# Optimization experiments

Measured on AMD Instinct MI355X. Metric: run time of the kernel, lower is better.

Reference implementation:

```python
import jax, jax.numpy as jnp
import numpy as np

B, T, F = 256, 288, 64
UNITS = [128, 64, 64, 32]
SCALE = 0.05  # small init so relu-activated recurrence stays numerically stable


def _lstm_scan(x_tbf, Wk, Wr, b):
    """Keras LSTM with activation=relu, recurrent_activation=sigmoid.
    x_tbf: [T, B, in]. Returns all hidden states [T, B, u].
    Gate order in the fused kernel is (i, f, g, o), as in Keras."""
    u = Wr.shape[0]
    bsz = x_tbf.shape[1]

    def step(carry, xt):
        h, c = carry
        z = xt @ Wk + h @ Wr + b            # [B, 4u]
        i, f, g, o = jnp.split(z, 4, axis=-1)
        i = jax.nn.sigmoid(i)
        f = jax.nn.sigmoid(f)
        g = jax.nn.relu(g)                   # cell-input activation = relu
        o = jax.nn.sigmoid(o)
        c = f * c + i * g
        h = o * jax.nn.relu(c)               # output activation = relu
        return (h, c), h

    init = (jnp.zeros((bsz, u), x_tbf.dtype), jnp.zeros((bsz, u), x_tbf.dtype))
    _, hs = jax.lax.scan(step, init, x_tbf)
    return hs  # [T, B, u]


def setup_inputs() -> dict:
    key = jax.random.key(0)
    ks = jax.random.split(key, 20)
    out = {"x": jax.random.normal(ks[0], (B, T, F), dtype=jnp.float32)}
    ins = [F] + UNITS[:-1]
    ki = 1
    for li, (din, u) in enumerate(zip(ins, UNITS), start=1):
        out[f"W{li}"] = jax.random.normal(ks[ki], (din, 4 * u), jnp.float32) * SCALE; ki += 1
        out[f"U{li}"] = jax.random.normal(ks[ki], (u, 4 * u), jnp.float32) * SCALE; ki += 1
        out[f"b{li}"] = jnp.zeros((4 * u,), jnp.float32)
    out["Wf"] = jax.random.normal(ks[ki], (UNITS[-1], 16), jnp.float32) * SCALE; ki += 1
    out["bf"] = jnp.zeros((16,), jnp.float32)
    out["Wo"] = jax.random.normal(ks[ki], (16, 1), jnp.float32) * SCALE
    out["bo"] = jnp.zeros((1,), jnp.float32)
    return out


def reference(x, W1, U1, b1, W2, U2, b2, W3, U3, b3, W4, U4, b4, Wf, bf, Wo, bo):
    # Dropout layers are identity at inference (Keras deterministic call).
    h = jnp.transpose(x, (1, 0, 2))          # [T, B, F] time-major for scan
    h = _lstm_scan(h, W1, U1, b1)            # [T, B, 128]
    h = _lstm_scan(h, W2, U2, b2)            # [T, B, 64]
    h = _lstm_scan(h, W3, U3, b3)            # [T, B, 64]
    h_last = _lstm_scan(h, W4, U4, b4)[-1]   # [B, 32] (return_sequences=False)
    fc = jax.nn.relu(h_last @ Wf + bf)       # [B, 16]
    return fc @ Wo + bo                      # [B, 1]
```

## Files before the change

kernel.cpp:

```cpp
#include <hip/hip_runtime.h>
#include <math.h>

#define TSTEPS 288
#define NTHREADS 512

typedef float f32x2 __attribute__((ext_vector_type(2)));

__device__ __forceinline__ float sigmoidf_(float x) {
    return 1.0f / (1.0f + __expf(-x));
}

__device__ __forceinline__ void pkfma(f32x2& acc, f32x2 w, f32x2 x) {
    asm("v_pk_fma_f32 %0, %1, %2, %0" : "+v"(acc) : "v"(w), "v"(x));
}

template<int NS>
__device__ __forceinline__ float allreduce_seg(float v) {
    if constexpr (NS > 1)
        v += __int_as_float(__builtin_amdgcn_update_dpp(
                0, __float_as_int(v), 0xB1, 0xF, 0xF, true));
    if constexpr (NS > 2)
        v += __int_as_float(__builtin_amdgcn_update_dpp(
                0, __float_as_int(v), 0x4E, 0xF, 0xF, true));
    if constexpr (NS > 4)
        v += __int_as_float(__builtin_amdgcn_ds_swizzle(
                __float_as_int(v), 0x101F));
    return v;
}

template<int NS, int KSEG>
__device__ __forceinline__ int perm_idx(int j) {
    return (((j % KSEG) >> 2) * NS + (j / KSEG)) * 4 + (j & 3);
}

__device__ void run_l1(const float* __restrict__ Wk, const float* __restrict__ Wr,
                       const float* __restrict__ bias, const float* __restrict__ xg,
                       float* __restrict__ seq, float* __restrict__ xh,
                       float* __restrict__ xring, int tid)
{
    constexpr int U = 128, COLS = 512, NPI = 8, NPH = 16, NP = NPI + NPH;
    const int seg = tid & 3;
    const int u   = tid >> 2;

    f32x2 w[4][NP];
#pragma unroll
    for (int q = 0; q < NPI; ++q) {
        const int k0 = seg * 16 + 2 * q;
#pragma unroll
        for (int g = 0; g < 4; ++g)
            w[g][q] = f32x2{Wk[(size_t)k0 * COLS + g * U + u],
                            Wk[(size_t)(k0 + 1) * COLS + g * U + u]};
    }
#pragma unroll
    for (int q = 0; q < NPH; ++q) {
        const int k0 = seg * 32 + 2 * q;
#pragma unroll
        for (int g = 0; g < 4; ++g)
            w[g][NPI + q] = f32x2{Wr[(size_t)k0 * COLS + g * U + u],
                                  Wr[(size_t)(k0 + 1) * COLS + g * U + u]};
    }
    float bz[4];
#pragma unroll
    for (int g = 0; g < 4; ++g) bz[g] = bias[g * U + u];
#pragma unroll
    for (int g = 0; g < 4; ++g)
#pragma unroll
        for (int q = 0; q < NP; ++q)
            asm volatile("" : "+v"(w[g][q]));

    float cst = 0.0f;

    for (int t = 0; t < TSTEPS; ++t) {
        const float* __restrict__ xr = xh + (t & 1) * 128;
        float* __restrict__ xw       = xh + ((t + 1) & 1) * 128;

        float xstage = 0.0f;
        if (tid < 64 && (t + 1) < TSTEPS) xstage = xg[(t + 1) * 64 + tid];

        f32x2 ac0 = {0.f,0.f}, ac1 = {0.f,0.f}, ac2 = {0.f,0.f}, ac3 = {0.f,0.f};

        {
            const float4* in4 = reinterpret_cast<const float4*>(xring + (t & 1) * 64) + seg;
#pragma unroll
            for (int k = 0; k < 4; ++k) {
                const float4 v = in4[k * 4];
                const f32x2 lo = {v.x, v.y}, hi = {v.z, v.w};
                pkfma(ac0, w[0][2*k],   lo); pkfma(ac0, w[0][2*k+1], hi);
                pkfma(ac1, w[1][2*k],   lo); pkfma(ac1, w[1][2*k+1], hi);
                pkfma(ac2, w[2][2*k],   lo); pkfma(ac2, w[2][2*k+1], hi);
                pkfma(ac3, w[3][2*k],   lo); pkfma(ac3, w[3][2*k+1], hi);
            }
        }
        {
            const float4* h4 = reinterpret_cast<const float4*>(xr) + seg;
#pragma unroll
            for (int k = 0; k < 8; ++k) {
                const float4 v = h4[k * 4];
                const f32x2 lo = {v.x, v.y}, hi = {v.z, v.w};
                const int pb = NPI + 2 * k;
                pkfma(ac0, w[0][pb], lo); pkfma(ac0, w[0][pb+1], hi);
                pkfma(ac1, w[1][pb], lo); pkfma(ac1, w[1][pb+1], hi);
                pkfma(ac2, w[2][pb], lo); pkfma(ac2, w[2][pb+1], hi);
                pkfma(ac3, w[3][pb], lo); pkfma(ac3, w[3][pb+1], hi);
            }
        }
        float a0 = allreduce_seg<4>(ac0[0] + ac0[1]) + bz[0];
        float a1 = allreduce_seg<4>(ac1[0] + ac1[1]) + bz[1];
        float a2 = allreduce_seg<4>(ac2[0] + ac2[1]) + bz[2];
        float a3 = allreduce_seg<4>(ac3[0] + ac3[1]) + bz[3];

        const float gi = sigmoidf_(a0);
        const float gf = sigmoidf_(a1);
        const float gg = fmaxf(a2, 0.0f);
        const float go = sigmoidf_(a3);
        cst = fmaf(gf, cst, gi * gg);
        const float h = go * fmaxf(cst, 0.0f);

        if (seg == 0) {
            const int pj = perm_idx<4, 32>(u);
            xw[pj] = h;
            seq[t * 128 + pj] = h;
        }
        if (tid < 64 && (t + 1) < TSTEPS)
            xring[((t + 1) & 1) * 64 + perm_idx<4, 16>(tid)] = xstage;
        __syncthreads();
    }
}

__device__ void fused_l2(const float* __restrict__ Wk, const float* __restrict__ Wr,
                         const float* __restrict__ bias,
                         const float* __restrict__ seq, float* __restrict__ xh2,
                         int lt)
{
    constexpr int U = 64, COLS = 256, NPI = 16, NPH = 8, NP = NPI + NPH;
    const int seg = lt & 3;
    const int u   = lt >> 2;

    f32x2 w[4][NP];
#pragma unroll
    for (int q = 0; q < NPI; ++q) {
        const int k0 = seg * 32 + 2 * q;
#pragma unroll
        for (int g = 0; g < 4; ++g)
            w[g][q] = f32x2{Wk[(size_t)k0 * COLS + g * U + u],
                            Wk[(size_t)(k0 + 1) * COLS + g * U + u]};
    }
#pragma unroll
    for (int q = 0; q < NPH; ++q) {
        const int k0 = seg * 16 + 2 * q;
#pragma unroll
        for (int g = 0; g < 4; ++g)
            w[g][NPI + q] = f32x2{Wr[(size_t)k0 * COLS + g * U + u],
                                  Wr[(size_t)(k0 + 1) * COLS + g * U + u]};
    }
    float bz[4];
#pragma unroll
    for (int g = 0; g < 4; ++g) bz[g] = bias[g * U + u];
#pragma unroll
    for (int g = 0; g < 4; ++g)
#pragma unroll
        for (int q = 0; q < NP; ++q)
            asm volatile("" : "+v"(w[g][q]));

    float cst = 0.0f;

    for (int i = 0; i < TSTEPS + 2; ++i) {
        if (i < TSTEPS) {
            f32x2 ac0 = {0.f,0.f}, ac1 = {0.f,0.f}, ac2 = {0.f,0.f}, ac3 = {0.f,0.f};
            {
                const float4* in4 = reinterpret_cast<const float4*>(seq + i * 128) + seg;
#pragma unroll
                for (int k = 0; k < 8; ++k) {
                    const float4 v = in4[k * 4];
                    const f32x2 lo = {v.x, v.y}, hi = {v.z, v.w};
                    pkfma(ac0, w[0][2*k],   lo); pkfma(ac0, w[0][2*k+1], hi);
                    pkfma(ac1, w[1][2*k],   lo); pkfma(ac1, w[1][2*k+1], hi);
                    pkfma(ac2, w[2][2*k],   lo); pkfma(ac2, w[2][2*k+1], hi);
                    pkfma(ac3, w[3][2*k],   lo); pkfma(ac3, w[3][2*k+1], hi);
                }
            }
            {
                const float4* h4 = reinterpret_cast<const float4*>(xh2 + ((i + 1) & 1) * 64) + seg;
#pragma unroll
                for (int k = 0; k < 4; ++k) {
                    const float4 v = h4[k * 4];
                    const f32x2 lo = {v.x, v.y}, hi = {v.z, v.w};
                    const int pb = NPI + 2 * k;
                    pkfma(ac0, w[0][pb], lo); pkfma(ac0, w[0][pb+1], hi);
                    pkfma(ac1, w[1][pb], lo); pkfma(ac1, w[1][pb+1], hi);
                    pkfma(ac2, w[2][pb], lo); pkfma(ac2, w[2][pb+1], hi);
                    pkfma(ac3, w[3][pb], lo); pkfma(ac3, w[3][pb+1], hi);
                }
            }
            float a0 = allreduce_seg<4>(ac0[0] + ac0[1]) + bz[0];
            float a1 = allreduce_seg<4>(ac1[0] + ac1[1]) + bz[1];
            float a2 = allreduce_seg<4>(ac2[0] + ac2[1]) + bz[2];
            float a3 = allreduce_seg<4>(ac3[0] + ac3[1]) + bz[3];

            const float gi = sigmoidf_(a0);
            const float gf = sigmoidf_(a1);
            const float gg = fmaxf(a2, 0.0f);
            const float go = sigmoidf_(a3);
            cst = fmaf(gf, cst, gi * gg);
            const float h = go * fmaxf(cst, 0.0f);

            if (seg == 0) xh2[(i & 1) * 64 + perm_idx<4, 16>(u)] = h;
        }
        __syncthreads();
    }
}

__device__ void fused_l34(const float* __restrict__ W3k, const float* __restrict__ W3r,
                          const float* __restrict__ b3,
                          const float* __restrict__ W4k, const float* __restrict__ W4r,
                          const float* __restrict__ b4,
                          const float* __restrict__ xh2, float* __restrict__ xh3,
                          float* __restrict__ xh4, int lt)
{
    const int seg3 = lt & 3,  u3 = lt >> 2;
    const int seg4 = lt & 7,  u4 = lt >> 3;

    f32x2 w3[4][16];
#pragma unroll
    for (int q = 0; q < 8; ++q) {
        const int k0 = seg3 * 16 + 2 * q;
#pragma unroll
        for (int g = 0; g < 4; ++g)
            w3[g][q] = f32x2{W3k[(size_t)k0 * 256 + g * 64 + u3],
                             W3k[(size_t)(k0 + 1) * 256 + g * 64 + u3]};
    }
#pragma unroll
    for (int q = 0; q < 8; ++q) {
        const int k0 = seg3 * 16 + 2 * q;
#pragma unroll
        for (int g = 0; g < 4; ++g)
            w3[g][8 + q] = f32x2{W3r[(size_t)k0 * 256 + g * 64 + u3],
                                 W3r[(size_t)(k0 + 1) * 256 + g * 64 + u3]};
    }
    f32x2 w4[4][6];
#pragma unroll
    for (int q = 0; q < 4; ++q) {
        const int k0 = seg4 * 8 + 2 * q;
#pragma unroll
        for (int g = 0; g < 4; ++g)
            w4[g][q] = f32x2{W4k[(size_t)k0 * 128 + g * 32 + u4],
                             W4k[(size_t)(k0 + 1) * 128 + g * 32 + u4]};
    }
#pragma unroll
    for (int q = 0; q < 2; ++q) {
        const int k0 = seg4 * 4 + 2 * q;
#pragma unroll
        for (int g = 0; g < 4; ++g)
            w4[g][4 + q] = f32x2{W4r[(size_t)k0 * 128 + g * 32 + u4],
                                 W4r[(size_t)(k0 + 1) * 128 + g * 32 + u4]};
    }
    float bz3[4], bz4[4];
#pragma unroll
    for (int g = 0; g < 4; ++g) { bz3[g] = b3[g * 64 + u3]; bz4[g] = b4[g * 32 + u4]; }
#pragma unroll
    for (int g = 0; g < 4; ++g) {
#pragma unroll
        for (int q = 0; q < 16; ++q) asm volatile("" : "+v"(w3[g][q]));
#pragma unroll
        for (int q = 0; q < 6;  ++q) asm volatile("" : "+v"(w4[g][q]));
    }

    float c3 = 0.0f, c4 = 0.0f;

    for (int i = 0; i < TSTEPS + 2; ++i) {
        if (i >= 1 && i <= TSTEPS) {
            f32x2 ac0 = {0.f,0.f}, ac1 = {0.f,0.f}, ac2 = {0.f,0.f}, ac3 = {0.f,0.f};
            {
                const float4* in4 = reinterpret_cast<const float4*>(xh2 + ((i - 1) & 1) * 64) + seg3;
#pragma unroll
                for (int k = 0; k < 4; ++k) {
                    const float4 v = in4[k * 4];
                    const f32x2 lo = {v.x, v.y}, hi = {v.z, v.w};
                    pkfma(ac0, w3[0][2*k],   lo); pkfma(ac0, w3[0][2*k+1], hi);
                    pkfma(ac1, w3[1][2*k],   lo); pkfma(ac1, w3[1][2*k+1], hi);
                    pkfma(ac2, w3[2][2*k],   lo); pkfma(ac2, w3[2][2*k+1], hi);
                    pkfma(ac3, w3[3][2*k],   lo); pkfma(ac3, w3[3][2*k+1], hi);
                }
            }
            {
                const float4* h4 = reinterpret_cast<const float4*>(xh3 + (i & 1) * 64) + seg3;
#pragma unroll
                for (int k = 0; k < 4; ++k) {
                    const float4 v = h4[k * 4];
                    const f32x2 lo = {v.x, v.y}, hi = {v.z, v.w};
                    const int pb = 8 + 2 * k;
                    pkfma(ac0, w3[0][pb], lo); pkfma(ac0, w3[0][pb+1], hi);
                    pkfma(ac1, w3[1][pb], lo); pkfma(ac1, w3[1][pb+1], hi);
                    pkfma(ac2, w3[2][pb], lo); pkfma(ac2, w3[2][pb+1], hi);
                    pkfma(ac3, w3[3][pb], lo); pkfma(ac3, w3[3][pb+1], hi);
                }
            }
            float a0 = allreduce_seg<4>(ac0[0] + ac0[1]) + bz3[0];
            float a1 = allreduce_seg<4>(ac1[0] + ac1[1]) + bz3[1];
            float a2 = allreduce_seg<4>(ac2[0] + ac2[1]) + bz3[2];
            float a3 = allreduce_seg<4>(ac3[0] + ac3[1]) + bz3[3];
            const float gi = sigmoidf_(a0);
            const float gf = sigmoidf_(a1);
            const float gg = fmaxf(a2, 0.0f);
            const float go = sigmoidf_(a3);
            c3 = fmaf(gf, c3, gi * gg);
            const float h = go * fmaxf(c3, 0.0f);
            if (seg3 == 0) xh3[((i - 1) & 1) * 64 + perm_idx<4, 16>(u3)] = h;
        }
        if (i >= 2) {
            f32x2 ac0 = {0.f,0.f}, ac1 = {0.f,0.f}, ac2 = {0.f,0.f}, ac3 = {0.f,0.f};
            {
                const float4* in4 = reinterpret_cast<const float4*>(xh3 + (i & 1) * 64);
#pragma unroll
                for (int k = 0; k < 2; ++k) {
                    const float4 v = in4[((seg4 & 1) * 2 + k) * 4 + (seg4 >> 1)];
                    const f32x2 lo = {v.x, v.y}, hi = {v.z, v.w};
                    pkfma(ac0, w4[0][2*k],   lo); pkfma(ac0, w4[0][2*k+1], hi);
                    pkfma(ac1, w4[1][2*k],   lo); pkfma(ac1, w4[1][2*k+1], hi);
                    pkfma(ac2, w4[2][2*k],   lo); pkfma(ac2, w4[2][2*k+1], hi);
                    pkfma(ac3, w4[3][2*k],   lo); pkfma(ac3, w4[3][2*k+1], hi);
                }
            }
            {
                const float4 v = reinterpret_cast<const float4*>(xh4 + ((i - 1) & 1) * 32)[seg4];
                const f32x2 lo = {v.x, v.y}, hi = {v.z, v.w};
                pkfma(ac0, w4[0][4], lo); pkfma(ac0, w4[0][5], hi);
                pkfma(ac1, w4[1][4], lo); pkfma(ac1, w4[1][5], hi);
                pkfma(ac2, w4[2][4], lo); pkfma(ac2, w4[2][5], hi);
                pkfma(ac3, w4[3][4], lo); pkfma(ac3, w4[3][5], hi);
            }
            float a0 = allreduce_seg<8>(ac0[0] + ac0[1]) + bz4[0];
            float a1 = allreduce_seg<8>(ac1[0] + ac1[1]) + bz4[1];
            float a2 = allreduce_seg<8>(ac2[0] + ac2[1]) + bz4[2];
            float a3 = allreduce_seg<8>(ac3[0] + ac3[1]) + bz4[3];
            const float gi = sigmoidf_(a0);
            const float gf = sigmoidf_(a1);
            const float gg = fmaxf(a2, 0.0f);
            const float go = sigmoidf_(a3);
            c4 = fmaf(gf, c4, gi * gg);
            const float h = go * fmaxf(c4, 0.0f);
            if (seg4 == 0) xh4[(i & 1) * 32 + u4] = h;
        }
        __syncthreads();
    }
}

extern "C" __global__ void __launch_bounds__(NTHREADS, 2)
lstm_stack_kernel(const float* __restrict__ x,
                  const float* __restrict__ W1, const float* __restrict__ U1, const float* __restrict__ b1,
                  const float* __restrict__ W2, const float* __restrict__ U2, const float* __restrict__ b2,
                  const float* __restrict__ W3, const float* __restrict__ U3, const float* __restrict__ b3,
                  const float* __restrict__ W4, const float* __restrict__ U4, const float* __restrict__ b4,
                  const float* __restrict__ Wf, const float* __restrict__ bf,
                  const float* __restrict__ Wo, const float* __restrict__ bo,
                  float* __restrict__ out)
{
    __shared__ __align__(16) float seq[TSTEPS * 128];
    __shared__ __align__(16) float xh1[2 * 128];
    __shared__ __align__(16) float xring[2 * 64];
    __shared__ __align__(16) float xh2[2 * 64];
    __shared__ __align__(16) float xh3[2 * 64];
    __shared__ __align__(16) float xh4[2 * 32];
    __shared__ __align__(16) float hbuf[16];

    const int tid = threadIdx.x;
    const float* xg = x + (size_t)blockIdx.x * TSTEPS * 64;

    if (tid < 128) xh1[tid] = 0.0f;
    if (tid < 64) {
        xring[perm_idx<4, 16>(tid)] = xg[tid];
        xh2[64 + tid] = 0.0f;
        xh3[64 + tid] = 0.0f;
    }
    if (tid < 32) xh4[32 + tid] = 0.0f;
    __syncthreads();

    run_l1(W1, U1, b1, xg, seq, xh1, xring, tid);

    if (tid < 256) fused_l2(W2, U2, b2, seq, xh2, tid);
    else           fused_l34(W3, U3, b3, W4, U4, b4, xh2, xh3, xh4, tid - 256);
    __syncthreads();

    if (tid < 16) {
        float acc = bf[tid];
#pragma unroll
        for (int k = 0; k < 32; ++k) acc = fmaf(xh4[32 + k], Wf[k * 16 + tid], acc);
        hbuf[tid] = fmaxf(acc, 0.0f);
    }
    __syncthreads();
    if (tid == 0) {
        float acc = bo[0];
#pragma unroll
        for (int k = 0; k < 16; ++k) acc = fmaf(hbuf[k], Wo[k], acc);
        out[blockIdx.x] = acc;
    }
}

extern "C" void kernel_launch(void* const* d_in, const int* in_sizes, int n_in,
                              void* d_out, int out_size, void* d_ws, size_t ws_size,
                              hipStream_t stream) {
    const float* x  = (const float*)d_in[0];
    const float* W1 = (const float*)d_in[1];
    const float* U1 = (const float*)d_in[2];
    const float* b1 = (const float*)d_in[3];
    const float* W2 = (const float*)d_in[4];
    const float* U2 = (const float*)d_in[5];
    const float* b2 = (const float*)d_in[6];
    const float* W3 = (const float*)d_in[7];
    const float* U3 = (const float*)d_in[8];
    const float* b3 = (const float*)d_in[9];
    const float* W4 = (const float*)d_in[10];
    const float* U4 = (const float*)d_in[11];
    const float* b4 = (const float*)d_in[12];
    const float* Wf = (const float*)d_in[13];
    const float* bf = (const float*)d_in[14];
    const float* Wo = (const float*)d_in[15];
    const float* bo = (const float*)d_in[16];
    float* out = (float*)d_out;

    lstm_stack_kernel<<<dim3(256), dim3(NTHREADS), 0, stream>>>(
        x, W1, U1, b1, W2, U2, b2, W3, U3, b3, W4, U4, b4, Wf, bf, Wo, bo, out);
}
```

Measured before the change: 576.2 us.

## Chunk input projections of layers 1-2 over four timesteps with prepacked weights

A prep kernel repacks W1 and W2 into a per-thread contiguous layout in workspace. The main kernel then computes the input-to-gate projection for four timesteps at once by streaming these weights from global/L2 instead of holding them in registers. Only the recurrent weights stay in registers, which frees VGPRs and takes the input projection out of the per-step critical path. The cost is repeated weight reads from memory each chunk, a larger x staging ring, and an extra kernel launch, with a fallback path kept for when workspace is too small.

```diff
diff --git a/kernel.cpp b/kernel.cpp
--- a/kernel.cpp
+++ b/kernel.cpp
@@ -33,181 +33,247 @@
     return (((j % KSEG) >> 2) * NS + (j / KSEG)) * 4 + (j & 3);
 }
 
-__device__ void run_l1(const float* __restrict__ Wk, const float* __restrict__ Wr,
-                       const float* __restrict__ bias, const float* __restrict__ xg,
-                       float* __restrict__ seq, float* __restrict__ xh,
-                       float* __restrict__ xring, int tid)
+extern "C" __global__ void prep_kernel(const float* __restrict__ W1,
+                                       const float* __restrict__ W2,
+                                       float* __restrict__ ws)
 {
-    constexpr int U = 128, COLS = 512, NPI = 8, NPH = 16, NP = NPI + NPH;
+    const int tid = threadIdx.x;
+    {
+        const int u = tid >> 2, seg = tid & 3;
+#pragma unroll
+        for (int g = 0; g < 4; ++g)
+#pragma unroll
+            for (int kk = 0; kk < 16; ++kk)
+                ws[tid * 64 + g * 16 + kk] = W1[(seg * 16 + kk) * 512 + g * 128 + u];
+    }
+    if (tid < 256) {
+        const int u = tid >> 2, seg = tid & 3;
+#pragma unroll
+        for (int g = 0; g < 4; ++g)
+#pragma unroll
+            for (int kk = 0; kk < 32; ++kk)
+                ws[32768 + tid * 128 + g * 32 + kk] = W2[(seg * 32 + kk) * 256 + g * 64 + u];
+    }
+}
+
+__device__ void run_l1_chunked(const float* __restrict__ U1w,
+                               const float* __restrict__ bias,
+                               const float* __restrict__ xg,
+                               const float* __restrict__ wsA,
+                               float* __restrict__ seq,
+                               float* __restrict__ xh,
+                               float* __restrict__ xring,
+                               int tid)
+{
     const int seg = tid & 3;
     const int u   = tid >> 2;
 
-    f32x2 w[4][NP];
-#pragma unroll
-    for (int q = 0; q < NPI; ++q) {
-        const int k0 = seg * 16 + 2 * q;
-#pragma unroll
-        for (int g = 0; g < 4; ++g)
-            w[g][q] = f32x2{Wk[(size_t)k0 * COLS + g * U + u],
-                            Wk[(size_t)(k0 + 1) * COLS + g * U + u]};
-    }
-#pragma unroll
-    for (int q = 0; q < NPH; ++q) {
-        const int k0 = seg * 32 + 2 * q;
-#pragma unroll
-        for (int g = 0; g < 4; ++g)
-            w[g][NPI + q] = f32x2{Wr[(size_t)k0 * COLS + g * U + u],
-                                  Wr[(size_t)(k0 + 1) * COLS + g * U + u]};
+    f32x2 wr[4][16];
+#pragma unroll
+    for (int q = 0; q < 16; ++q) {
+        const int row = seg * 32 + 2 * q;
+#pragma unroll
+        for (int g = 0; g < 4; ++g)
+            wr[g][q] = f32x2{U1w[(size_t)row * 512 + g * 128 + u],
+                             U1w[(size_t)(row + 1) * 512 + g * 128 + u]};
     }
     float bz[4];
 #pragma unroll
-    for (int g = 0; g < 4; ++g) bz[g] = bias[g * U + u];
+    for (int g = 0; g < 4; ++g) bz[g] = bias[g * 128 + u];
 #pragma unroll
     for (int g = 0; g < 4; ++g)
 #pragma unroll
-        for (int q = 0; q < NP; ++q)
-            asm volatile("" : "+v"(w[g][q]));
+        for (int q = 0; q < 16; ++q)
+            asm volatile("" : "+v"(wr[g][q]));
+
+    if (tid < 128) xh[tid] = 0.0f;
+    if (tid < 256) {
+        const int r = tid >> 6, c = tid & 63;
+        xring[r * 64 + c] = xg[r * 64 + c];
+    }
+    __syncthreads();
 
     float cst = 0.0f;
-
-    for (int t = 0; t < TSTEPS; ++t) {
-        const float* __restrict__ xr = xh + (t & 1) * 128;
-        float* __restrict__ xw       = xh + ((t + 1) & 1) * 128;
-
-        float xstage = 0.0f;
-        if (tid < 64 && (t + 1) < TSTEPS) xstage = xg[(t + 1) * 64 + tid];
-
-        f32x2 ac0 = {0.f,0.f}, ac1 = {0.f,0.f}, ac2 = {0.f,0.f}, ac3 = {0.f,0.f};
-
+    const float4* wA = reinterpret_cast<const float4*>(wsA) + tid * 16;
+
+    for (int cc = 0; cc < 72; ++cc) {
+        float zx[4][4];
         {
-            const float4* in4 = reinterpret_cast<const float4*>(xring + (t & 1) * 64) + seg;
-#pragma unroll
-            for (int k = 0; k < 4; ++k) {
-                const float4 v = in4[k * 4];
-                const f32x2 lo = {v.x, v.y}, hi = {v.z, v.w};
-                pkfma(ac0, w[0][2*k],   lo); pkfma(ac0, w[0][2*k+1], hi);
-                pkfma(ac1, w[1][2*k],   lo); pkfma(ac1, w[1][2*k+1], hi);
-                pkfma(ac2, w[2][2*k],   lo); pkfma(ac2, w[2][2*k+1], hi);
-                pkfma(ac3, w[3][2*k],   lo); pkfma(ac3, w[3][2*k+1], hi);
-            }
-        }
-        {
+            const float4* xr4 = reinterpret_cast<const float4*>(xring + (cc & 1) * 256);
+            f32x2 acc2[4][4];
+#pragma unroll
+            for (int t = 0; t < 4; ++t)
+#pragma unroll
+                for (int g = 0; g < 4; ++g) acc2[t][g] = f32x2{0.f, 0.f};
+
+#pragma unroll
+            for (int g = 0; g < 4; ++g) {
+                const float4 w0 = wA[g * 4 + 0], w1 = wA[g * 4 + 1],
+                             w2 = wA[g * 4 + 2], w3 = wA[g * 4 + 3];
+#pragma unroll
+                for (int t = 0; t < 4; ++t) {
+                    const float4 x0 = xr4[t * 16 + seg * 4 + 0];
+                    const float4 x1 = xr4[t * 16 + seg * 4 + 1];
+                    const float4 x2 = xr4[t * 16 + seg * 4 + 2];
+                    const float4 x3 = xr4[t * 16 + seg * 4 + 3];
+                    pkfma(acc2[t][g], f32x2{w0.x, w0.y}, f32x2{x0.x, x0.y});
+                    pkfma(acc2[t][g], f32x2{w0.z, w0.w}, f32x2{x0.z, x0.w});
+                    pkfma(acc2[t][g], f32x2{w1.x, w1.y}, f32x2{x1.x, x1.y});
+                    pkfma(acc2[t][g], f32x2{w1.z, w1.w}, f32x2{x1.z, x1.w});
+                    pkfma(acc2[t][g], f32x2{w2.x, w2.y}, f32x2{x2.x, x2.y});
+                    pkfma(acc2[t][g], f32x2{w2.z, w2.w}, f32x2{x2.z, x2.w});
+                    pkfma(acc2[t][g], f32x2{w3.x, w3.y}, f32x2{x3.x, x3.y});
+                    pkfma(acc2[t][g], f32x2{w3.z, w3.w}, f32x2{x3.z, x3.w});
+                }
+            }
+#pragma unroll
+            for (int t = 0; t < 4; ++t)
+#pragma unroll
+                for (int g = 0; g < 4; ++g)
+                    zx[t][g] = allreduce_seg<4>(acc2[t][g][0] + acc2[t][g][1]);
+        }
+
+#pragma unroll
+        for (int tp = 0; tp < 4; ++tp) {
+            const int t = cc * 4 + tp;
+            const float* __restrict__ xr = xh + (t & 1) * 128;
+            float* __restrict__ xw       = xh + ((t + 1) & 1) * 128;
+
+            f32x2 a2[4] = {f32x2{0.f,0.f}, f32x2{0.f,0.f}, f32x2{0.f,0.f}, f32x2{0.f,0.f}};
             const float4* h4 = reinterpret_cast<const float4*>(xr) + seg;
 #pragma unroll
             for (int k = 0; k < 8; ++k) {
                 const float4 v = h4[k * 4];
                 const f32x2 lo = {v.x, v.y}, hi = {v.z, v.w};
-                const int pb = NPI + 2 * k;
-                pkfma(ac0, w[0][pb], lo); pkfma(ac0, w[0][pb+1], hi);
-                pkfma(ac1, w[1][pb], lo); pkfma(ac1, w[1][pb+1], hi);
-                pkfma(ac2, w[2][pb], lo); pkfma(ac2, w[2][pb+1], hi);
-                pkfma(ac3, w[3][pb], lo); pkfma(ac3, w[3][pb+1], hi);
-            }
-        }
-        float a0 = allreduce_seg<4>(ac0[0] + ac0[1]) + bz[0];
-        float a1 = allreduce_seg<4>(ac1[0] + ac1[1]) + bz[1];
-        float a2 = allreduce_seg<4>(ac2[0] + ac2[1]) + bz[2];
-        float a3 = allreduce_seg<4>(ac3[0] + ac3[1]) + bz[3];
-
-        const float gi = sigmoidf_(a0);
-        const float gf = sigmoidf_(a1);
-        const float gg = fmaxf(a2, 0.0f);
-        const float go = sigmoidf_(a3);
-        cst = fmaf(gf, cst, gi * gg);
-        const float h = go * fmaxf(cst, 0.0f);
-
-        if (seg == 0) {
-            const int pj = perm_idx<4, 32>(u);
-            xw[pj] = h;
-            seq[t * 128 + pj] = h;
-        }
-        if (tid < 64 && (t + 1) < TSTEPS)
-            xring[((t + 1) & 1) * 64 + perm_idx<4, 16>(tid)] = xstage;
-        __syncthreads();
-    }
-}
-
-__device__ void fused_l2(const float* __restrict__ Wk, const float* __restrict__ Wr,
-                         const float* __restrict__ bias,
-                         const float* __restrict__ seq, float* __restrict__ xh2,
-                         int lt)
+                pkfma(a2[0], wr[0][2*k], lo); pkfma(a2[0], wr[0][2*k+1], hi);
+                pkfma(a2[1], wr[1][2*k], lo); pkfma(a2[1], wr[1][2*k+1], hi);
+                pkfma(a2[2], wr[2][2*k], lo); pkfma(a2[2], wr[2][2*k+1], hi);
+                pkfma(a2[3], wr[3][2*k], lo); pkfma(a2[3], wr[3][2*k+1], hi);
+            }
+            float a[4];
+#pragma unroll
+            for (int g = 0; g < 4; ++g)
+                a[g] = allreduce_seg<4>(a2[g][0] + a2[g][1]) + zx[tp][g] + bz[g];
+
+            const float gi = sigmoidf_(a[0]);
+            const float gf = sigmoidf_(a[1]);
+            const float gg = fmaxf(a[2], 0.0f);
+            const float go = sigmoidf_(a[3]);
+            cst = fmaf(gf, cst, gi * gg);
+            const float h = go * fmaxf(cst, 0.0f);
+
+            if (seg == 0) {
+                const int pj = perm_idx<4, 32>(u);
+                xw[pj] = h;
+                seq[t * 128 + pj] = h;
+            }
+            if (tp == 0 && tid < 256) {
+                const int r = (cc + 1) * 4 + (tid >> 6), c = tid & 63;
+                if (r < TSTEPS)
+                    xring[((cc + 1) & 1) * 256 + (tid >> 6) * 64 + c] = xg[r * 64 + c];
+            }
+            __syncthreads();
+        }
+    }
+}
+
+__device__ void fused_l2c(const float* __restrict__ U2w,
+                          const float* __restrict__ bias,
+                          const float* __restrict__ wsB,
+                          const float* __restrict__ seq,
+                          float* __restrict__ xh2,
+                          int lt)
 {
-    constexpr int U = 64, COLS = 256, NPI = 16, NPH = 8, NP = NPI + NPH;
     const int seg = lt & 3;
     const int u   = lt >> 2;
 
-    f32x2 w[4][NP];
-#pragma unroll
-    for (int q = 0; q < NPI; ++q) {
-        const int k0 = seg * 32 + 2 * q;
-#pragma unroll
-        for (int g = 0; g < 4; ++g)
-            w[g][q] = f32x2{Wk[(size_t)k0 * COLS + g * U + u],
-                            Wk[(size_t)(k0 + 1) * COLS + g * U + u]};
-    }
-#pragma unroll
-    for (int q = 0; q < NPH; ++q) {
-        const int k0 = seg * 16 + 2 * q;
-#pragma unroll
-        for (int g = 0; g < 4; ++g)
-            w[g][NPI + q] = f32x2{Wr[(size_t)k0 * COLS + g * U + u],
-                                  Wr[(size_t)(k0 + 1) * COLS + g * U + u]};
+    f32x2 wr[4][8];
+#pragma unroll
+    for (int q = 0; q < 8; ++q) {
+        const int row = seg * 16 + 2 * q;
+#pragma unroll
+        for (int g = 0; g < 4; ++g)
+            wr[g][q] = f32x2{U2w[(size_t)row * 256 + g * 64 + u],
+                             U2w[(size_t)(row + 1) * 256 + g * 64 + u]};
     }
     float bz[4];
 #pragma unroll
-    for (int g = 0; g < 4; ++g) bz[g] = bias[g * U + u];
+    for (int g = 0; g < 4; ++g) bz[g] = bias[g * 64 + u];
 #pragma unroll
     for (int g = 0; g < 4; ++g)
 #pragma unroll
-        for (int q = 0; q < NP; ++q)
-            asm volatile("" : "+v"(w[g][q]));
+        for (int q = 0; q < 8; ++q)
+            asm volatile("" : "+v"(wr[g][q]));
 
     float cst = 0.0f;
-
-    for (int i = 0; i < TSTEPS + 2; ++i) {
-        if (i < TSTEPS) {
-            f32x2 ac0 = {0.f,0.f}, ac1 = {0.f,0.f}, ac2 = {0.f,0.f}, ac3 = {0.f,0.f};
-            {
-                const float4* in4 = reinterpret_cast<const float4*>(seq + i * 128) + seg;
-#pragma unroll
-                for (int k = 0; k < 8; ++k) {
-                    const float4 v = in4[k * 4];
-                    const f32x2 lo = {v.x, v.y}, hi = {v.z, v.w};
-                    pkfma(ac0, w[0][2*k],   lo); pkfma(ac0, w[0][2*k+1], hi);
-                    pkfma(ac1, w[1][2*k],   lo); pkfma(ac1, w[1][2*k+1], hi);
-                    pkfma(ac2, w[2][2*k],   lo); pkfma(ac2, w[2][2*k+1], hi);
-                    pkfma(ac3, w[3][2*k],   lo); pkfma(ac3, w[3][2*k+1], hi);
+    const float4* wB = reinterpret_cast<const float4*>(wsB) + lt * 32;
+
+    for (int cc = 0; cc < 72; ++cc) {
+        float zx[4][4];
+        {
+            f32x2 acc2[4][4];
+#pragma unroll
+            for (int t = 0; t < 4; ++t)
+#pragma unroll
+                for (int g = 0; g < 4; ++g) acc2[t][g] = f32x2{0.f, 0.f};
+
+#pragma unroll
+            for (int g = 0; g < 4; ++g) {
+                float4 wv[8];
+#pragma unroll
+                for (int n = 0; n < 8; ++n) wv[n] = wB[g * 8 + n];
+#pragma unroll
+                for (int t = 0; t < 4; ++t) {
+                    const float4* in4 = reinterpret_cast<const float4*>(
+                        seq + (cc * 4 + t) * 128) + seg;
+#pragma unroll
+                    for (int n = 0; n < 8; ++n) {
+                        const float4 v = in4[n * 4];
+                        pkfma(acc2[t][g], f32x2{wv[n].x, wv[n].y}, f32x2{v.x, v.y});
+                        pkfma(acc2[t][g], f32x2{wv[n].z, wv[n].w}, f32x2{v.z, v.w});
+                    }
                 }
             }
-            {
-                const float4* h4 = reinterpret_cast<const float4*>(xh2 + ((i + 1) & 1) * 64) + seg;
-#pragma unroll
-                for (int k = 0; k < 4; ++k) {
-                    const float4 v = h4[k * 4];
-                    const f32x2 lo = {v.x, v.y}, hi = {v.z, v.w};
-                    const int pb = NPI + 2 * k;
-                    pkfma(ac0, w[0][pb], lo); pkfma(ac0, w[0][pb+1], hi);
-                    pkfma(ac1, w[1][pb], lo); pkfma(ac1, w[1][pb+1], hi);
-                    pkfma(ac2, w[2][pb], lo); pkfma(ac2, w[2][pb+1], hi);
-                    pkfma(ac3, w[3][pb], lo); pkfma(ac3, w[3][pb+1], hi);
-                }
-            }
-            float a0 = allreduce_seg<4>(ac0[0] + ac0[1]) + bz[0];
-            float a1 = allreduce_seg<4>(ac1[0] + ac1[1]) + bz[1];
-            float a2 = allreduce_seg<4>(ac2[0] + ac2[1]) + bz[2];
-            float a3 = allreduce_seg<4>(ac3[0] + ac3[1]) + bz[3];
-
-            const float gi = sigmoidf_(a0);
-            const float gf = sigmoidf_(a1);
-            const float gg = fmaxf(a2, 0.0f);
-            const float go = sigmoidf_(a3);
+#pragma unroll
+            for (int t = 0; t < 4; ++t)
+#pragma unroll
+                for (int g = 0; g < 4; ++g)
+                    zx[t][g] = allreduce_seg<4>(acc2[t][g][0] + acc2[t][g][1]);
+        }
+
+#pragma unroll
+        for (int tp = 0; tp < 4; ++tp) {
+            const int i = cc * 4 + tp;
+            f32x2 a2[4] = {f32x2{0.f,0.f}, f32x2{0.f,0.f}, f32x2{0.f,0.f}, f32x2{0.f,0.f}};
+            const float4* h4 = reinterpret_cast<const float4*>(
+                xh2 + ((i + 1) & 1) * 64) + seg;
+#pragma unroll
+            for (int k = 0; k < 4; ++k) {
+                const float4 v = h4[k * 4];
+                const f32x2 lo = {v.x, v.y}, hi = {v.z, v.w};
+                pkfma(a2[0], wr[0][2*k], lo); pkfma(a2[0], wr[0][2*k+1], hi);
+                pkfma(a2[1], wr[1][2*k], lo); pkfma(a2[1], wr[1][2*k+1], hi);
+                pkfma(a2[2], wr[2][2*k], lo); pkfma(a2[2], wr[2][2*k+1], hi);
+                pkfma(a2[3], wr[3][2*k], lo); pkfma(a2[3], wr[3][2*k+1], hi);
+            }
+            float a[4];
+#pragma unroll
+            for (int g = 0; g < 4; ++g)
+                a[g] = allreduce_seg<4>(a2[g][0] + a2[g][1]) + zx[tp][g] + bz[g];
+
+            const float gi = sigmoidf_(a[0]);
+            const float gf = sigmoidf_(a[1]);
+            const float gg = fmaxf(a[2], 0.0f);
+            const float go = sigmoidf_(a[3]);
             cst = fmaf(gf, cst, gi * gg);
             const float h = go * fmaxf(cst, 0.0f);
 
             if (seg == 0) xh2[(i & 1) * 64 + perm_idx<4, 16>(u)] = h;
-        }
-        __syncthreads();
-    }
+            __syncthreads();
+        }
+    }
+    __syncthreads();
+    __syncthreads();
 }
 
 __device__ void fused_l34(const float* __restrict__ W3k, const float* __restrict__ W3r,
@@ -346,14 +412,237 @@
 }
 
 extern "C" __global__ void __launch_bounds__(NTHREADS, 2)
-lstm_stack_kernel(const float* __restrict__ x,
-                  const float* __restrict__ W1, const float* __restrict__ U1, const float* __restrict__ b1,
-                  const float* __restrict__ W2, const float* __restrict__ U2, const float* __restrict__ b2,
-                  const float* __restrict__ W3, const float* __restrict__ U3, const float* __restrict__ b3,
-                  const float* __restrict__ W4, const float* __restrict__ U4, const float* __restrict__ b4,
-                  const float* __restrict__ Wf, const float* __restrict__ bf,
-                  const float* __restrict__ Wo, const float* __restrict__ bo,
-                  float* __restrict__ out)
+lstm_fast_kernel(const float* __restrict__ x,
+                 const float* __restrict__ U1, const float* __restrict__ b1,
+                 const float* __restrict__ U2, const float* __restrict__ b2,
+                 const float* __restrict__ W3, const float* __restrict__ U3, const float* __restrict__ b3,
+                 const float* __restrict__ W4, const float* __restrict__ U4, const float* __restrict__ b4,
+                 const float* __restrict__ Wf, const float* __restrict__ bf,
+                 const float* __restrict__ Wo, const float* __restrict__ bo,
+                 const float* __restrict__ ws,
+                 float* __restrict__ out)
+{
+    __shared__ __align__(16) float seq[TSTEPS * 128];
+    __shared__ __align__(16) float xh1[2 * 128];
+    __shared__ __align__(16) float xring[2 * 256];
+    __shared__ __align__(16) float xh2[2 * 64];
+    __shared__ __align__(16) float xh3[2 * 64];
+    __shared__ __align__(16) float xh4[2 * 32];
+    __shared__ __align__(16) float hbuf[16];
+
+    const int tid = threadIdx.x;
+    const float* xg = x + (size_t)blockIdx.x * TSTEPS * 64;
+
+    if (tid < 64) { xh2[64 + tid] = 0.0f; xh3[64 + tid] = 0.0f; }
+    if (tid < 32) xh4[32 + tid] = 0.0f;
+
+    run_l1_chunked(U1, b1, xg, ws, seq, xh1, xring, tid);
+    __syncthreads();
+
+    if (tid < 256) fused_l2c(U2, b2, ws + 32768, seq, xh2, tid);
+    else           fused_l34(W3, U3, b3, W4, U4, b4, xh2, xh3, xh4, tid - 256);
+    __syncthreads();
+
+    if (tid < 16) {
+        float acc = bf[tid];
+#pragma unroll
+        for (int k = 0; k < 32; ++k) acc = fmaf(xh4[32 + k], Wf[k * 16 + tid], acc);
+        hbuf[tid] = fmaxf(acc, 0.0f);
+    }
+    __syncthreads();
+    if (tid == 0) {
+        float acc = bo[0];
+#pragma unroll
+        for (int k = 0; k < 16; ++k) acc = fmaf(hbuf[k], Wo[k], acc);
+        out[blockIdx.x] = acc;
+    }
+}
+
+__device__ void run_l1_fb(const float* __restrict__ Wk, const float* __restrict__ Wr,
+                          const float* __restrict__ bias, const float* __restrict__ xg,
+                          float* __restrict__ seq, float* __restrict__ xh,
+                          float* __restrict__ xring, int tid)
+{
+    constexpr int U = 128, COLS = 512, NPI = 8, NPH = 16, NP = NPI + NPH;
+    const int seg = tid & 3;
+    const int u   = tid >> 2;
+
+    f32x2 w[4][NP];
+#pragma unroll
+    for (int q = 0; q < NPI; ++q) {
+        const int k0 = seg * 16 + 2 * q;
+#pragma unroll
+        for (int g = 0; g < 4; ++g)
+            w[g][q] = f32x2{Wk[(size_t)k0 * COLS + g * U + u],
+                            Wk[(size_t)(k0 + 1) * COLS + g * U + u]};
+    }
+#pragma unroll
+    for (int q = 0; q < NPH; ++q) {
+        const int k0 = seg * 32 + 2 * q;
+#pragma unroll
+        for (int g = 0; g < 4; ++g)
+            w[g][NPI + q] = f32x2{Wr[(size_t)k0 * COLS + g * U + u],
+                                  Wr[(size_t)(k0 + 1) * COLS + g * U + u]};
+    }
+    float bz[4];
+#pragma unroll
+    for (int g = 0; g < 4; ++g) bz[g] = bias[g * U + u];
+#pragma unroll
+    for (int g = 0; g < 4; ++g)
+#pragma unroll
+        for (int q = 0; q < NP; ++q)
+            asm volatile("" : "+v"(w[g][q]));
+
+    float cst = 0.0f;
+
+    for (int t = 0; t < TSTEPS; ++t) {
+        const float* __restrict__ xr = xh + (t & 1) * 128;
+        float* __restrict__ xw       = xh + ((t + 1) & 1) * 128;
+
+        float xstage = 0.0f;
+        if (tid < 64 && (t + 1) < TSTEPS) xstage = xg[(t + 1) * 64 + tid];
+
+        f32x2 ac0 = {0.f,0.f}, ac1 = {0.f,0.f}, ac2 = {0.f,0.f}, ac3 = {0.f,0.f};
+        {
+            const float4* in4 = reinterpret_cast<const float4*>(xring + (t & 1) * 64) + seg;
+#pragma unroll
+            for (int k = 0; k < 4; ++k) {
+                const float4 v = in4[k * 4];
+                const f32x2 lo = {v.x, v.y}, hi = {v.z, v.w};
+                pkfma(ac0, w[0][2*k],   lo); pkfma(ac0, w[0][2*k+1], hi);
+                pkfma(ac1, w[1][2*k],   lo); pkfma(ac1, w[1][2*k+1], hi);
+                pkfma(ac2, w[2][2*k],   lo); pkfma(ac2, w[2][2*k+1], hi);
+                pkfma(ac3, w[3][2*k],   lo); pkfma(ac3, w[3][2*k+1], hi);
+            }
+        }
+        {
+            const float4* h4 = reinterpret_cast<const float4*>(xr) + seg;
+#pragma unroll
+            for (int k = 0; k < 8; ++k) {
+                const float4 v = h4[k * 4];
+                const f32x2 lo = {v.x, v.y}, hi = {v.z, v.w};
+                const int pb = NPI + 2 * k;
+                pkfma(ac0, w[0][pb], lo); pkfma(ac0, w[0][pb+1], hi);
+                pkfma(ac1, w[1][pb], lo); pkfma(ac1, w[1][pb+1], hi);
+                pkfma(ac2, w[2][pb], lo); pkfma(ac2, w[2][pb+1], hi);
+                pkfma(ac3, w[3][pb], lo); pkfma(ac3, w[3][pb+1], hi);
+            }
+        }
+        float a0 = allreduce_seg<4>(ac0[0] + ac0[1]) + bz[0];
+        float a1 = allreduce_seg<4>(ac1[0] + ac1[1]) + bz[1];
+        float a2 = allreduce_seg<4>(ac2[0] + ac2[1]) + bz[2];
+        float a3 = allreduce_seg<4>(ac3[0] + ac3[1]) + bz[3];
+
+        const float gi = sigmoidf_(a0);
+        const float gf = sigmoidf_(a1);
+        const float gg = fmaxf(a2, 0.0f);
+        const float go = sigmoidf_(a3);
+        cst = fmaf(gf, cst, gi * gg);
+        const float h = go * fmaxf(cst, 0.0f);
+
+        if (seg == 0) {
+            const int pj = perm_idx<4, 32>(u);
+            xw[pj] = h;
+            seq[t * 128 + pj] = h;
+        }
+        if (tid < 64 && (t + 1) < TSTEPS)
+            xring[((t + 1) & 1) * 64 + perm_idx<4, 16>(tid)] = xstage;
+        __syncthreads();
+    }
+}
+
+__device__ void fused_l2_fb(const float* __restrict__ Wk, const float* __restrict__ Wr,
+                            const float* __restrict__ bias,
+                            const float* __restrict__ seq, float* __restrict__ xh2,
+                            int lt)
+{
+    constexpr int U = 64, COLS = 256, NPI = 16, NPH = 8, NP = NPI + NPH;
+    const int seg = lt & 3;
+    const int u   = lt >> 2;
+
+    f32x2 w[4][NP];
+#pragma unroll
+    for (int q = 0; q < NPI; ++q) {
+        const int k0 = seg * 32 + 2 * q;
+#pragma unroll
+        for (int g = 0; g < 4; ++g)
+            w[g][q] = f32x2{Wk[(size_t)k0 * COLS + g * U + u],
+                            Wk[(size_t)(k0 + 1) * COLS + g * U + u]};
+    }
+#pragma unroll
+    for (int q = 0; q < NPH; ++q) {
+        const int k0 = seg * 16 + 2 * q;
+#pragma unroll
+        for (int g = 0; g < 4; ++g)
+            w[g][NPI + q] = f32x2{Wr[(size_t)k0 * COLS + g * U + u],
+                                  Wr[(size_t)(k0 + 1) * COLS + g * U + u]};
+    }
+    float bz[4];
+#pragma unroll
+    for (int g = 0; g < 4; ++g) bz[g] = bias[g * U + u];
+#pragma unroll
+    for (int g = 0; g < 4; ++g)
+#pragma unroll
+        for (int q = 0; q < NP; ++q)
+            asm volatile("" : "+v"(w[g][q]));
+
+    float cst = 0.0f;
+
+    for (int i = 0; i < TSTEPS + 2; ++i) {
+        if (i < TSTEPS) {
+            f32x2 ac0 = {0.f,0.f}, ac1 = {0.f,0.f}, ac2 = {0.f,0.f}, ac3 = {0.f,0.f};
+            {
+                const float4* in4 = reinterpret_cast<const float4*>(seq + i * 128) + seg;
+#pragma unroll
+                for (int k = 0; k < 8; ++k) {
+                    const float4 v = in4[k * 4];
+                    const f32x2 lo = {v.x, v.y}, hi = {v.z, v.w};
+                    pkfma(ac0, w[0][2*k],   lo); pkfma(ac0, w[0][2*k+1], hi);
+                    pkfma(ac1, w[1][2*k],   lo); pkfma(ac1, w[1][2*k+1], hi);
+                    pkfma(ac2, w[2][2*k],   lo); pkfma(ac2, w[2][2*k+1], hi);
+                    pkfma(ac3, w[3][2*k],   lo); pkfma(ac3, w[3][2*k+1], hi);
+                }
+            }
+            {
+                const float4* h4 = reinterpret_cast<const float4*>(xh2 + ((i + 1) & 1) * 64) + seg;
+#pragma unroll
+                for (int k = 0; k < 4; ++k) {
+                    const float4 v = h4[k * 4];
+                    const f32x2 lo = {v.x, v.y}, hi = {v.z, v.w};
+                    const int pb = NPI + 2 * k;
+                    pkfma(ac0, w[0][pb], lo); pkfma(ac0, w[0][pb+1], hi);
+                    pkfma(ac1, w[1][pb], lo); pkfma(ac1, w[1][pb+1], hi);
+                    pkfma(ac2, w[2][pb], lo); pkfma(ac2, w[2][pb+1], hi);
+                    pkfma(ac3, w[3][pb], lo); pkfma(ac3, w[3][pb+1], hi);
+                }
+            }
+            float a0 = allreduce_seg<4>(ac0[0] + ac0[1]) + bz[0];
+            float a1 = allreduce_seg<4>(ac1[0] + ac1[1]) + bz[1];
+            float a2 = allreduce_seg<4>(ac2[0] + ac2[1]) + bz[2];
+            float a3 = allreduce_seg<4>(ac3[0] + ac3[1]) + bz[3];
+
+            const float gi = sigmoidf_(a0);
+            const float gf = sigmoidf_(a1);
+            const float gg = fmaxf(a2, 0.0f);
+            const float go = sigmoidf_(a3);
+            cst = fmaf(gf, cst, gi * gg);
+            const float h = go * fmaxf(cst, 0.0f);
+
+            if (seg == 0) xh2[(i & 1) * 64 + perm_idx<4, 16>(u)] = h;
+        }
+        __syncthreads();
+    }
+}
+
+extern "C" __global__ void __launch_bounds__(NTHREADS, 2)
+lstm_fallback_kernel(const float* __restrict__ x,
+                     const float* __restrict__ W1, const float* __restrict__ U1, const float* __restrict__ b1,
+                     const float* __restrict__ W2, const float* __restrict__ U2, const float* __restrict__ b2,
+                     const float* __restrict__ W3, const float* __restrict__ U3, const float* __restrict__ b3,
+                     const float* __restrict__ W4, const float* __restrict__ U4, const float* __restrict__ b4,
+                     const float* __restrict__ Wf, const float* __restrict__ bf,
+                     const float* __restrict__ Wo, const float* __restrict__ bo,
+                     float* __restrict__ out)
 {
     __shared__ __align__(16) float seq[TSTEPS * 128];
     __shared__ __align__(16) float xh1[2 * 128];
@@ -375,9 +664,9 @@
     if (tid < 32) xh4[32 + tid] = 0.0f;
     __syncthreads();
 
-    run_l1(W1, U1, b1, xg, seq, xh1, xring, tid);
-
-    if (tid < 256) fused_l2(W2, U2, b2, seq, xh2, tid);
+    run_l1_fb(W1, U1, b1, xg, seq, xh1, xring, tid);
+
+    if (tid < 256) fused_l2_fb(W2, U2, b2, seq, xh2, tid);
     else           fused_l34(W3, U3, b3, W4, U4, b4, xh2, xh3, xh4, tid - 256);
     __syncthreads();
 
@@ -418,6 +707,13 @@
     const float* bo = (const float*)d_in[16];
     float* out = (float*)d_out;
 
-    lstm_stack_kernel<<<dim3(256), dim3(NTHREADS), 0, stream>>>(
-        x, W1, U1, b1, W2, U2, b2, W3, U3, b3, W4, U4, b4, Wf, bf, Wo, bo, out);
-}
+    if (ws_size >= 65536 * sizeof(float)) {
+        prep_kernel<<<dim3(1), dim3(512), 0, stream>>>(W1, W2, (float*)d_ws);
+        lstm_fast_kernel<<<dim3(256), dim3(NTHREADS), 0, stream>>>(
+            x, U1, b1, U2, b2, W3, U3, b3, W4, U4, b4, Wf, bf, Wo, bo,
+            (const float*)d_ws, out);
+    } else {
+        lstm_fallback_kernel<<<dim3(256), dim3(NTHREADS), 0, stream>>>(
+            x, W1, U1, b1, W2, U2, b2, W3, U3, b3, W4, U4, b4, Wf, bf, Wo, bo, out);
+    }
+}
```

Result: slower. 997.6 us (+73.1%).
